# Kernel tuning notes

Hardware: AMD Instinct MI355X
Metric: run time of the kernel (lower is better)

Reference implementation:

```python
import jax, jax.numpy as jnp
import numpy as np
from jax import lax

B, IN_C, H, W = 2, 256, 80, 80
OUT_C = 256
INTER = IN_C // 16          # 16
C4 = IN_C // 4              # 64
K = 3
DIL = [7, 5, 2, 1]
PADS = [(K + (K - 1) * (d - 1)) // 2 for d in DIL]  # same-padding per module formula


def conv2d(x, w, b=None, pad=0, dil=1, groups=1):
    out = lax.conv_general_dilated(
        x, w, (1, 1), [(pad, pad), (pad, pad)], rhs_dilation=(dil, dil),
        dimension_numbers=('NCHW', 'OIHW', 'NCHW'), feature_group_count=groups)
    if b is not None:
        out = out + b[None, :, None, None]
    return out


def bnorm(x, g, b, eps=1e-3):
    # BatchNorm2d in training mode (fresh module): biased batch stats, eps=0.001
    m = x.mean((0, 2, 3), keepdims=True)
    v = x.var((0, 2, 3), keepdims=True)
    return (x - m) * lax.rsqrt(v + eps) * g[None, :, None, None] + b[None, :, None, None]


def gnorm(x, g, b, groups=4, eps=1e-5):
    Bb, C, Hh, Ww = x.shape
    xr = x.reshape(Bb, groups, C // groups, Hh, Ww)
    m = xr.mean((2, 3, 4), keepdims=True)
    v = xr.var((2, 3, 4), keepdims=True)
    xr = (xr - m) * lax.rsqrt(v + eps)
    return xr.reshape(Bb, C, Hh, Ww) * g[None, :, None, None] + b[None, :, None, None]


def setup_inputs() -> dict:
    keys = jax.random.split(jax.random.key(0), 40)

    def w_init(k, shape):
        fan = float(np.prod(shape[1:]))
        return jax.random.normal(k, shape, jnp.float32) / np.sqrt(fan)

    d = {}
    d['z'] = jax.random.normal(keys[0], (B, IN_C, H, W), jnp.float32)
    for i in range(4):  # depthwise dilated convs: (C4, 1, 3, 3)
        d[f'w_at{i}'] = w_init(keys[1 + 2 * i], (C4, 1, K, K))
        d[f'b_at{i}'] = jax.random.normal(keys[2 + 2 * i], (C4,), jnp.float32) * 0.02
    d['gn_w'] = 1.0 + 0.05 * jax.random.normal(keys[9], (IN_C,), jnp.float32)
    d['gn_b'] = 0.05 * jax.random.normal(keys[10], (IN_C,), jnp.float32)
    d['conv_w'] = w_init(keys[11], (IN_C, IN_C, 1, 1))
    d['conv_b'] = jax.random.normal(keys[12], (IN_C,), jnp.float32) * 0.02
    d['c5a_w'] = w_init(keys[13], (INTER, IN_C, 3, 3))
    d['bn5a_w'] = 1.0 + 0.05 * jax.random.normal(keys[14], (INTER,), jnp.float32)
    d['bn5a_b'] = 0.05 * jax.random.normal(keys[15], (INTER,), jnp.float32)
    d['c5c_w'] = w_init(keys[16], (INTER, IN_C, 3, 3))
    d['bn5c_w'] = 1.0 + 0.05 * jax.random.normal(keys[17], (INTER,), jnp.float32)
    d['bn5c_b'] = 0.05 * jax.random.normal(keys[18], (INTER,), jnp.float32)
    d['pq_w'] = w_init(keys[19], (INTER // 8, INTER, 1, 1))
    d['pq_b'] = jax.random.normal(keys[20], (INTER // 8,), jnp.float32) * 0.02
    d['pk_w'] = w_init(keys[21], (INTER // 8, INTER, 1, 1))
    d['pk_b'] = jax.random.normal(keys[22], (INTER // 8,), jnp.float32) * 0.02
    d['pv_w'] = w_init(keys[23], (INTER, INTER, 1, 1))
    d['pv_b'] = jax.random.normal(keys[24], (INTER,), jnp.float32) * 0.02
    d['pa_gamma'] = 0.5 * jnp.ones((1,), jnp.float32)  # nonzero so attn path is exercised
    d['ca_gamma'] = 0.5 * jnp.ones((1,), jnp.float32)
    d['c5b_w'] = w_init(keys[25], (INTER, INTER, 3, 3))
    d['bn5b_w'] = 1.0 + 0.05 * jax.random.normal(keys[26], (INTER,), jnp.float32)
    d['bn5b_b'] = 0.05 * jax.random.normal(keys[27], (INTER,), jnp.float32)
    d['c5d_w'] = w_init(keys[28], (INTER, INTER, 3, 3))
    d['bn5d_w'] = 1.0 + 0.05 * jax.random.normal(keys[29], (INTER,), jnp.float32)
    d['bn5d_b'] = 0.05 * jax.random.normal(keys[30], (INTER,), jnp.float32)
    d['c6_w'] = w_init(keys[31], (OUT_C, INTER, 1, 1))
    d['c6_b'] = jax.random.normal(keys[32], (OUT_C,), jnp.float32) * 0.02
    return d


def reference(z, w_at0, b_at0, w_at1, b_at1, w_at2, b_at2, w_at3, b_at3,
              gn_w, gn_b, conv_w, conv_b,
              c5a_w, bn5a_w, bn5a_b, c5c_w, bn5c_w, bn5c_b,
              pq_w, pq_b, pk_w, pk_b, pv_w, pv_b, pa_gamma, ca_gamma,
              c5b_w, bn5b_w, bn5b_b, c5d_w, bn5d_w, bn5d_b, c6_w, c6_b):
    parts = jnp.split(z, 4, axis=1)
    ws = [w_at0, w_at1, w_at2, w_at3]
    bs = [b_at0, b_at1, b_at2, b_at3]
    zs = [conv2d(parts[i], ws[i], bs[i], pad=PADS[i], dil=DIL[i], groups=C4)
          for i in range(4)]
    zc = jnp.concatenate(zs, axis=1)
    zc = jax.nn.gelu(conv2d(gnorm(zc, gn_w, gn_b), conv_w, conv_b), approximate=False)

    # --- DABlock ---
    feat1 = jax.nn.relu(bnorm(conv2d(zc, c5a_w, pad=1), bn5a_w, bn5a_b))
    Bb, C, Hh, Ww = feat1.shape
    N = Hh * Ww
    # PAM: full HWxHW attention
    q = conv2d(feat1, pq_w, pq_b).reshape(Bb, -1, N)   # (B, C//8, N)
    k = conv2d(feat1, pk_w, pk_b).reshape(Bb, -1, N)
    v = conv2d(feat1, pv_w, pv_b).reshape(Bb, C, N)
    energy = jnp.einsum('bcn,bcm->bnm', q, k)          # (B, N, N)
    att = jax.nn.softmax(energy, axis=-1)
    pa = jnp.einsum('bcm,bnm->bcn', v, att).reshape(Bb, C, Hh, Ww)
    pa = pa_gamma * pa + feat1
    pa_conv = jax.nn.relu(bnorm(conv2d(pa, c5b_w, pad=1), bn5b_w, bn5b_b))

    feat2 = jax.nn.relu(bnorm(conv2d(zc, c5c_w, pad=1), bn5c_w, bn5c_b))
    # CAM: CxC attention
    xf = feat2.reshape(Bb, C, N)
    e = jnp.einsum('bcn,bdn->bcd', xf, xf)             # (B, C, C)
    e = e.max(-1, keepdims=True) - e
    att_c = jax.nn.softmax(e, axis=-1)
    ca = jnp.einsum('bcd,bdn->bcn', att_c, xf).reshape(Bb, C, Hh, Ww)
    ca = ca_gamma * ca + feat2
    ca_conv = jax.nn.relu(bnorm(conv2d(ca, c5d_w, pad=1), bn5d_w, bn5d_b))

    # Dropout2d(p=0.05) is identity in eval mode
    out = jax.nn.relu(conv2d(pa_conv + ca_conv, c6_w, c6_b))
    return out
```

## Files before the change

### kernel.cpp

```cpp
#include <hip/hip_runtime.h>
#include <math.h>

#define HW 6400

typedef __attribute__((ext_vector_type(8))) short bf16x8;
typedef __attribute__((ext_vector_type(4))) float f32x4;

__device__ __forceinline__ float wredsum(float v){
  #pragma unroll
  for (int o = 32; o; o >>= 1) v += __shfl_xor(v, o);
  return v;
}

__device__ __forceinline__ unsigned short f2bf(float f){
  unsigned int u = __float_as_uint(f);
  u += 0x7FFF + ((u >> 16) & 1);
  return (unsigned short)(u >> 16);
}

__device__ __forceinline__ float bf2f(unsigned short s){
  return __uint_as_float((unsigned int)s << 16);
}

__device__ __forceinline__ unsigned int cvt_pk_bf16(float lo, float hi){
  unsigned int r;
  asm("v_cvt_pk_bf16_f32 %0, %1, %2" : "=v"(r) : "v"(lo), "v"(hi));
  return r;
}

__device__ __forceinline__ float gelu(float v){
  return 0.5f * v * (1.f + erff(v * 0.70710678118f));
}

__global__ __launch_bounds__(256) void k_prep(
    const float* __restrict__ wa, const float* __restrict__ wc,
    const float* __restrict__ wb, const float* __restrict__ wd,
    const float* __restrict__ cw, const float* __restrict__ gn_sc,
    const float* __restrict__ cb,
    unsigned short* __restrict__ wbbf,
    unsigned short* __restrict__ cwbf, float* __restrict__ cbp,
    unsigned short* __restrict__ wbbf2){
  int bx = blockIdx.x;
  int tid = threadIdx.x;
  if (bx < 288){
    int i = bx * 256 + tid;
    if (i < 73728){
      int j = i & 7, l = (i >> 3) & 63, f = (i >> 9) & 1, ss = i >> 10;
      int k = ss * 32 + (l >> 4) * 8 + j;
      int off = k >> 8, ic = k & 255;
      int oc = f * 16 + (l & 15);
      float v = (oc < 16) ? wa[(oc * 256 + ic) * 9 + off]
                          : wc[((oc - 16) * 256 + ic) * 9 + off];
      wbbf[i] = f2bf(v);
    }
  } else if (bx < 800){
    int i = (bx - 288) * 256 + tid;
    int b = i >> 16, r = i & 65535;
    int j = r & 7, l = (r >> 3) & 63, f = (r >> 9) & 15, ss = r >> 13;
    int ic = ss * 32 + (l >> 4) * 8 + j;
    int oc = f * 16 + (l & 15);
    cwbf[i] = f2bf(cw[oc * 256 + ic] * gn_sc[(b * 256 + ic) * 2]);
  } else if (bx < 832){
    int bb = bx - 800;
    int b = bb >> 4;
    int oc = (bb & 15) * 16 + (tid >> 4);
    int cp = tid & 15;
    float s2 = 0.f;
    #pragma unroll
    for (int k = 0; k < 16; k++){
      int c = cp * 16 + k;
      s2 += cw[oc * 256 + c] * gn_sc[(b * 256 + c) * 2 + 1];
    }
    s2 += __shfl_xor(s2, 1); s2 += __shfl_xor(s2, 2);
    s2 += __shfl_xor(s2, 4); s2 += __shfl_xor(s2, 8);
    if (cp == 0) cbp[b * 256 + oc] = cb[oc] + s2;
  } else {
    int i = (bx - 832) * 256 + tid;
    if (i < 9216){
      int j = i & 7, l = (i >> 3) & 63, f = (i >> 9) & 1, off = i >> 10;
      int kk = (l >> 4) * 8 + j;
      int oc = f * 16 + (l & 15);
      float v = 0.f;
      if (oc < 16 && kk < 16)        v = wb[(oc * 16 + kk) * 9 + off];
      else if (oc >= 16 && kk >= 16) v = wd[((oc - 16) * 16 + (kk - 16)) * 9 + off];
      wbbf2[i] = f2bf(v);
    }
  }
}

__global__ __launch_bounds__(256) void k_dwt(
    const float* __restrict__ z,
    const float* __restrict__ w0, const float* __restrict__ b0,
    const float* __restrict__ w1, const float* __restrict__ b1,
    const float* __restrict__ w2, const float* __restrict__ b2,
    const float* __restrict__ w3, const float* __restrict__ b3,
    unsigned short* __restrict__ zbf, float* __restrict__ gnpart){
  __shared__ unsigned short lt[64][66];
  int tid = threadIdx.x;
  int g = blockIdx.y, b = blockIdx.z;
  int p0 = blockIdx.x * 64;
  int lane = tid & 63, s = tid >> 6;
  int pix = p0 + lane;
  int h = pix / 80, w = pix % 80;
  const float* wp; const float* bp; int d;
  if (g == 0){ wp = w0; bp = b0; d = 7; }
  else if (g == 1){ wp = w1; bp = b1; d = 5; }
  else if (g == 2){ wp = w2; bp = b2; d = 2; }
  else            { wp = w3; bp = b3; d = 1; }
  int offr[9]; float msk[9];
  #pragma unroll
  for (int kh = 0; kh < 3; kh++){
    #pragma unroll
    for (int kw = 0; kw < 3; kw++){
      bool ok = ((unsigned)(h + (kh - 1) * d) < 80u) && ((unsigned)(w + (kw - 1) * d) < 80u);
      offr[kh * 3 + kw] = ok ? ((kh - 1) * d * 80 + (kw - 1) * d) : 0;
      msk[kh * 3 + kw] = ok ? 1.f : 0.f;
    }
  }
  const float* zb = z + (size_t)(b * 256 + g * 64) * HW + pix;
  for (int j = 0; j < 16; j++){
    int cl = s * 16 + j;
    const float* zin = zb + (size_t)cl * HW;
    const float* wr = wp + cl * 9;
    float acc = bp[cl];
    #pragma unroll
    for (int k = 0; k < 9; k++) acc = fmaf(wr[k], zin[offr[k]] * msk[k], acc);
    float S = wredsum(acc), Q = wredsum(acc * acc);
    if (lane == 0){
      int cg = b * 256 + g * 64 + cl;
      gnpart[(cg * 100 + blockIdx.x) * 2]     = S;
      gnpart[(cg * 100 + blockIdx.x) * 2 + 1] = Q;
    }
    lt[lane][cl] = f2bf(acc);
  }
  __syncthreads();
  int pr = tid >> 2, q = tid & 3;
  const unsigned short* src = &lt[pr][q * 16];
  unsigned int tmp[8];
  #pragma unroll
  for (int u = 0; u < 8; u++) tmp[u] = *(const unsigned int*)(src + u * 2);
  uint4 v0 = make_uint4(tmp[0], tmp[1], tmp[2], tmp[3]);
  uint4 v1 = make_uint4(tmp[4], tmp[5], tmp[6], tmp[7]);
  unsigned short* dst = zbf + ((size_t)b * HW + p0 + pr) * 256 + g * 64 + q * 16;
  *(uint4*)dst = v0;
  *(uint4*)(dst + 8) = v1;
}

__global__ __launch_bounds__(256) void k_gnfin(
    const float* __restrict__ gnpart, const float* __restrict__ gn_w,
    const float* __restrict__ gn_b, float* __restrict__ gn_sc){
  int tid = threadIdx.x; int bg = blockIdx.x;
  int b = bg >> 2, g = bg & 3;
  size_t base = (size_t)(b * 256 + g * 64) * 200;
  float S = 0.f, Q = 0.f;
  for (int i = tid; i < 6400; i += 256){
    S += gnpart[base + 2 * i];
    Q += gnpart[base + 2 * i + 1];
  }
  S = wredsum(S); Q = wredsum(Q);
  __shared__ float l[8];
  int lane = tid & 63, wid = tid >> 6;
  if (lane == 0){ l[wid] = S; l[4 + wid] = Q; }
  __syncthreads();
  float SS = l[0] + l[1] + l[2] + l[3];
  float QQ = l[4] + l[5] + l[6] + l[7];
  float M = 64.f * HW;
  float mean = SS / M;
  float var = QQ / M - mean * mean;
  float rstd = rsqrtf(var + 1e-5f);
  if (tid < 64){
    int c = g * 64 + tid;
    float sc = gn_w[c] * rstd;
    float sh = gn_b[c] - mean * sc;
    gn_sc[(b * 256 + c) * 2] = sc;
    gn_sc[(b * 256 + c) * 2 + 1] = sh;
  }
}

__global__ __launch_bounds__(256) void k_conv1_mfma(
    const unsigned short* __restrict__ zbf,
    const unsigned short* __restrict__ cwbf,
    const float* __restrict__ cbp,
    unsigned short* __restrict__ zbfT){
  __shared__ __align__(16) unsigned char lmem[64 * 512];
  unsigned short* lda = (unsigned short*)lmem;
  unsigned short* lout = (unsigned short*)lmem;
  int tid = threadIdx.x;
  int p0 = blockIdx.x * 64, ocg = blockIdx.y, b = blockIdx.z;
  #pragma unroll
  for (int k = 0; k < 8; k++){
    int m = tid + k * 256;
    int i = m >> 5, c = m & 31;
    bf16x8 val = *(const bf16x8*)(zbf + ((size_t)b * HW + p0 + i) * 256 + c * 8);
    *(bf16x8*)(lda + i * 256 + (c ^ (i & 7)) * 8) = val;
  }
  __syncthreads();
  int wv = tid >> 6, l = tid & 63;
  int row = l & 15, kg = l >> 4;
  int i = wv * 16 + row;
  f32x4 acc0 = {0.f,0.f,0.f,0.f}, acc1 = {0.f,0.f,0.f,0.f};
  f32x4 acc2 = {0.f,0.f,0.f,0.f}, acc3 = {0.f,0.f,0.f,0.f};
  const unsigned short* wp = cwbf + (size_t)b * 65536 + (ocg * 4) * 512 + l * 8;
  #pragma unroll
  for (int s = 0; s < 8; s++){
    int c = s * 4 + kg;
    bf16x8 a = *(const bf16x8*)(lda + i * 256 + (c ^ (i & 7)) * 8);
    const unsigned short* wps = wp + s * 8192;
    bf16x8 b0 = *(const bf16x8*)(wps);
    bf16x8 b1 = *(const bf16x8*)(wps + 512);
    bf16x8 b2 = *(const bf16x8*)(wps + 1024);
    bf16x8 b3 = *(const bf16x8*)(wps + 1536);
    acc0 = __builtin_amdgcn_mfma_f32_16x16x32_bf16(a, b0, acc0, 0, 0, 0);
    acc1 = __builtin_amdgcn_mfma_f32_16x16x32_bf16(a, b1, acc1, 0, 0, 0);
    acc2 = __builtin_amdgcn_mfma_f32_16x16x32_bf16(a, b2, acc2, 0, 0, 0);
    acc3 = __builtin_amdgcn_mfma_f32_16x16x32_bf16(a, b3, acc3, 0, 0, 0);
  }
  __syncthreads();
  const float* cbb = cbp + b * 256 + ocg * 64;
  int oc_l = l & 15;
  int pl = wv * 16 + kg * 4;
  float bs0 = cbb[oc_l], bs1 = cbb[16 + oc_l], bs2 = cbb[32 + oc_l], bs3 = cbb[48 + oc_l];
  #pragma unroll
  for (int r = 0; r < 4; r++){
    lout[(pl + r) * 72 + oc_l]      = f2bf(gelu(acc0[r] + bs0));
    lout[(pl + r) * 72 + 16 + oc_l] = f2bf(gelu(acc1[r] + bs1));
    lout[(pl + r) * 72 + 32 + oc_l] = f2bf(gelu(acc2[r] + bs2));
    lout[(pl + r) * 72 + 48 + oc_l] = f2bf(gelu(acc3[r] + bs3));
  }
  __syncthreads();
  int pix = tid >> 2, q = tid & 3;
  unsigned short* dst = zbfT + ((size_t)b * HW + p0 + pix) * 256 + ocg * 64 + q * 16;
  const unsigned short* src = lout + pix * 72 + q * 16;
  *(uint4*)dst       = *(const uint4*)src;
  *(uint4*)(dst + 8) = *(const uint4*)(src + 8);
}

__device__ __forceinline__ void c5_gload(bf16x8* r, const unsigned short* zbase,
    int p0, int irow, int c31, const int* hh, const int* ww, int off){
  int dy = off / 3 - 1, dx = off % 3 - 1;
  int doff = dy * 80 + dx;
  #pragma unroll
  for (int k = 0; k < 8; k++){
    int op = p0 + irow + k * 8;
    bool v = ((unsigned)(hh[k] + dy) < 80u) && ((unsigned)(ww[k] + dx) < 80u);
    int sp = v ? (op + doff) : op;
    bf16x8 val = *(const bf16x8*)(zbase + (size_t)sp * 256 + c31 * 8);
    if (!v) val = (bf16x8){0, 0, 0, 0, 0, 0, 0, 0};
    r[k] = val;
  }
}

__global__ __launch_bounds__(256) void k_conv5ac2(
    const unsigned short* __restrict__ zbfT,
    const unsigned short* __restrict__ wbbf,
    float* __restrict__ fpre, float* __restrict__ bnpart){
  __shared__ __align__(16) unsigned short lda[2][64 * 256];
  int tid = threadIdx.x;
  int och = blockIdx.y, b = blockIdx.z;
  int p0 = blockIdx.x * 64;
  int irow = tid >> 5, c31 = tid & 31;
  int hh[8], ww[8];
  #pragma unroll
  for (int k = 0; k < 8; k++){
    int op = p0 + irow + k * 8;
    hh[k] = op / 80; ww[k] = op % 80;
  }
  const unsigned short* zbase = zbfT + (size_t)b * HW * 256;
  bf16x8 r[8];
  c5_gload(r, zbase, p0, irow, c31, hh, ww, 0);
  #pragma unroll
  for (int k = 0; k < 8; k++){
    int i = irow + k * 8;
    *(bf16x8*)(lda[0] + i * 256 + (c31 ^ (i & 7)) * 8) = r[k];
  }
  c5_gload(r, zbase, p0, irow, c31, hh, ww, 1);
  int wv = tid >> 6, l = tid & 63;
  int lrow = l & 15, kg = l >> 4;
  int li = wv * 16 + lrow;
  f32x4 acc = {0.f, 0.f, 0.f, 0.f};
  for (int off = 0; off < 9; off++){
    __syncthreads();
    int buf = off & 1;
    const unsigned short* wp = wbbf + (size_t)off * 8192 + och * 512 + l * 8;
    #pragma unroll
    for (int s = 0; s < 8; s++){
      int cc = s * 4 + kg;
      bf16x8 a = *(const bf16x8*)(lda[buf] + li * 256 + (cc ^ (li & 7)) * 8);
      bf16x8 bb = *(const bf16x8*)(wp + s * 1024);
      acc = __builtin_amdgcn_mfma_f32_16x16x32_bf16(a, bb, acc, 0, 0, 0);
    }
    if (off + 1 < 9){
      #pragma unroll
      for (int k = 0; k < 8; k++){
        int i = irow + k * 8;
        *(bf16x8*)(lda[buf ^ 1] + i * 256 + (c31 ^ (i & 7)) * 8) = r[k];
      }
      if (off + 2 < 9) c5_gload(r, zbase, p0, irow, c31, hh, ww, off + 2);
    }
  }
  __syncthreads();
  float* lout = (float*)lda;
  int ocl = l & 15;
  int pl = wv * 16 + kg * 4;
  #pragma unroll
  for (int rr = 0; rr < 4; rr++) lout[ocl * 68 + pl + rr] = acc[rr];
  __syncthreads();
  int oc = tid >> 4, px = (tid & 15) * 4;
  float4 v = *(float4*)(lout + oc * 68 + px);
  *(float4*)(fpre + ((size_t)(b * 32 + och * 16 + oc)) * HW + p0 + px) = v;
  float S = v.x + v.y + v.z + v.w;
  float Q = v.x * v.x + v.y * v.y + v.z * v.z + v.w * v.w;
  #pragma unroll
  for (int o2 = 1; o2 < 16; o2 <<= 1){ S += __shfl_xor(S, o2); Q += __shfl_xor(Q, o2); }
  if ((tid & 15) == 0){
    int ocg = och * 16 + oc;
    bnpart[ocg * 400 + (b * 100 + blockIdx.x) * 2]     = S;
    bnpart[ocg * 400 + (b * 100 + blockIdx.x) * 2 + 1] = Q;
  }
}

__global__ __launch_bounds__(256) void k_featqkv(
    const float* __restrict__ fpre, const float* __restrict__ bnpart,
    const float* __restrict__ w1, const float* __restrict__ b1,
    const float* __restrict__ w2, const float* __restrict__ b2,
    const float* __restrict__ pqw, const float* __restrict__ pqb,
    const float* __restrict__ pkw, const float* __restrict__ pkb,
    const float* __restrict__ pvw, const float* __restrict__ pvb,
    float* __restrict__ feat, float* __restrict__ qkvT,
    float* __restrict__ cam_part){
  __shared__ float lS[8][32], lQ[8][32], lsc[64];
  __shared__ float lf2[256][17];
  int tid = threadIdx.x; int b = blockIdx.y;
  {
    int oc = tid & 31, sl = tid >> 5;
    float S = 0.f, Q = 0.f;
    for (int i = sl; i < 200; i += 8){
      S += bnpart[oc * 400 + i * 2];
      Q += bnpart[oc * 400 + i * 2 + 1];
    }
    lS[sl][oc] = S; lQ[sl][oc] = Q;
    __syncthreads();
    if (tid < 32){
      float SS = 0.f, QQ = 0.f;
      #pragma unroll
      for (int s = 0; s < 8; s++){ SS += lS[s][tid]; QQ += lQ[s][tid]; }
      float M = 2.f * HW;
      float mean = SS / M, var = QQ / M - mean * mean;
      float rstd = rsqrtf(var + 1e-3f);
      float w  = (tid < 16) ? w1[tid] : w2[tid - 16];
      float bb = (tid < 16) ? b1[tid] : b2[tid - 16];
      float sc = w * rstd;
      lsc[tid * 2] = sc; lsc[tid * 2 + 1] = bb - mean * sc;
    }
    __syncthreads();
  }
  int n = blockIdx.x * 256 + tid;
  float f1[16], f2[16];
  #pragma unroll
  for (int c = 0; c < 16; c++){
    float v1 = fpre[(b * 32 + c) * HW + n] * lsc[c * 2] + lsc[c * 2 + 1];
    f1[c] = fmaxf(v1, 0.f);
    float v2 = fpre[(b * 32 + 16 + c) * HW + n] * lsc[(16 + c) * 2] + lsc[(16 + c) * 2 + 1];
    f2[c] = fmaxf(v2, 0.f);
    feat[(b * 32 + c) * HW + n] = f1[c];
    feat[(b * 32 + 16 + c) * HW + n] = f2[c];
    lf2[tid][c] = f2[c];
  }
  float* o = qkvT + ((size_t)b * HW + n) * 20;
  #pragma unroll
  for (int j = 0; j < 2; j++){
    float q = pqb[j], k = pkb[j];
    #pragma unroll
    for (int c = 0; c < 16; c++){ q += pqw[j * 16 + c] * f1[c]; k += pkw[j * 16 + c] * f1[c]; }
    o[j] = q; o[2 + j] = k;
  }
  #pragma unroll
  for (int j = 0; j < 16; j++){
    float v = pvb[j];
    #pragma unroll
    for (int c = 0; c < 16; c++) v += pvw[j * 16 + c] * f1[c];
    o[4 + j] = v;
  }
  __syncthreads();
  int cc = tid >> 4, dd = tid & 15;
  float s = 0.f;
  #pragma unroll 4
  for (int p = 0; p < 256; p++) s = fmaf(lf2[p][cc], lf2[p][dd], s);
  cam_part[((size_t)blockIdx.x * 2 + b) * 256 + tid] = s;
}

__global__ __launch_bounds__(256) void k_pam_a(
    const float* __restrict__ qkvT, float* __restrict__ part){
  __shared__ __align__(16) float lk0[800];
  __shared__ __align__(16) float lk1[800];
  __shared__ __align__(16) unsigned short lvb[16][808];
  __shared__ float lred[4];
  int tid = threadIdx.x;
  int mc = blockIdx.y, b = blockIdx.z;
  float sqm = 0.f;
  for (int m = tid; m < 800; m += 256){
    const float* kv = qkvT + ((size_t)b * HW + mc * 800 + m) * 20;
    float4 a0 = *(const float4*)kv;
    lk0[m] = a0.z; lk1[m] = a0.w;
    sqm = fmaxf(sqm, a0.z * a0.z + a0.w * a0.w);
    float4 v0 = *(const float4*)(kv + 4);
    float4 v1 = *(const float4*)(kv + 8);
    float4 v2 = *(const float4*)(kv + 12);
    float4 v3 = *(const float4*)(kv + 16);
    lvb[0][m]  = f2bf(v0.x); lvb[1][m]  = f2bf(v0.y);
    lvb[2][m]  = f2bf(v0.z); lvb[3][m]  = f2bf(v0.w);
    lvb[4][m]  = f2bf(v1.x); lvb[5][m]  = f2bf(v1.y);
    lvb[6][m]  = f2bf(v1.z); lvb[7][m]  = f2bf(v1.w);
    lvb[8][m]  = f2bf(v2.x); lvb[9][m]  = f2bf(v2.y);
    lvb[10][m] = f2bf(v2.z); lvb[11][m] = f2bf(v2.w);
    lvb[12][m] = f2bf(v3.x); lvb[13][m] = f2bf(v3.y);
    lvb[14][m] = f2bf(v3.z); lvb[15][m] = f2bf(v3.w);
  }
  #pragma unroll
  for (int o = 32; o; o >>= 1) sqm = fmaxf(sqm, __shfl_xor(sqm, o));
  int lane = tid & 63, wid = tid >> 6;
  if (lane == 0) lred[wid] = sqm;
  __syncthreads();
  float kmax = sqrtf(fmaxf(fmaxf(lred[0], lred[1]), fmaxf(lred[2], lred[3])));
  int wv = tid >> 6, l = tid & 63;
  int row = l & 15, kg = l >> 4;
  int n = blockIdx.x * 64 + wv * 16 + row;
  const float* qp = qkvT + ((size_t)b * HW + n) * 20;
  float q0 = qp[0], q1 = qp[1];
  float mxr = sqrtf(q0 * q0 + q1 * q1) * kmax;
  f32x4 acc = {0.f, 0.f, 0.f, 0.f};
  float zp = 0.f;
  for (int t = 0; t < 25; t++){
    int m0 = t * 32 + kg * 8;
    float4 k0a = *(const float4*)&lk0[m0];
    float4 k0b = *(const float4*)&lk0[m0 + 4];
    float4 k1a = *(const float4*)&lk1[m0];
    float4 k1b = *(const float4*)&lk1[m0 + 4];
    float p0 = __expf(fmaf(q0, k0a.x, q1 * k1a.x) - mxr);
    float p1 = __expf(fmaf(q0, k0a.y, q1 * k1a.y) - mxr);
    float p2 = __expf(fmaf(q0, k0a.z, q1 * k1a.z) - mxr);
    float p3 = __expf(fmaf(q0, k0a.w, q1 * k1a.w) - mxr);
    float p4 = __expf(fmaf(q0, k0b.x, q1 * k1b.x) - mxr);
    float p5 = __expf(fmaf(q0, k0b.y, q1 * k1b.y) - mxr);
    float p6 = __expf(fmaf(q0, k0b.z, q1 * k1b.z) - mxr);
    float p7 = __expf(fmaf(q0, k0b.w, q1 * k1b.w) - mxr);
    zp += ((p0 + p1) + (p2 + p3)) + ((p4 + p5) + (p6 + p7));
    union { unsigned int u[4]; bf16x8 v; } pk;
    pk.u[0] = cvt_pk_bf16(p0, p1);
    pk.u[1] = cvt_pk_bf16(p2, p3);
    pk.u[2] = cvt_pk_bf16(p4, p5);
    pk.u[3] = cvt_pk_bf16(p6, p7);
    bf16x8 vb = *(const bf16x8*)&lvb[row][m0];
    acc = __builtin_amdgcn_mfma_f32_16x16x32_bf16(pk.v, vb, acc, 0, 0, 0);
  }
  zp += __shfl_xor(zp, 16);
  zp += __shfl_xor(zp, 32);
  float* pp = part + ((size_t)(b * 8 + mc) * 18) * HW;
  if (kg == 0){ pp[n] = mxr; pp[HW + n] = zp; }
  int c = l & 15;
  int nr = blockIdx.x * 64 + wv * 16 + (l >> 4) * 4;
  *(f32x4*)&pp[(size_t)(2 + c) * HW + nr] = acc;
}

__global__ __launch_bounds__(256) void k_merge(
    const float* __restrict__ part, const float* __restrict__ feat,
    const float* __restrict__ cam_part,
    const float* __restrict__ pa_g, const float* __restrict__ ca_g,
    unsigned short* __restrict__ mc){
  __shared__ float le[256];
  __shared__ float lsm[8][16];
  int tid = threadIdx.x; int y = blockIdx.y, b = blockIdx.z;
  int n = blockIdx.x * 256 + tid;
  union { unsigned short s[8]; uint4 u; } rowo;
  if (y < 2){
    int c0 = y * 8;
    float mxs[8]; float mx = -1e30f;
    #pragma unroll
    for (int m8 = 0; m8 < 8; m8++){
      mxs[m8] = part[((size_t)(b * 8 + m8) * 18) * HW + n];
      mx = fmaxf(mx, mxs[m8]);
    }
    float Z = 0.f, a[8];
    #pragma unroll
    for (int j = 0; j < 8; j++) a[j] = 0.f;
    #pragma unroll
    for (int m8 = 0; m8 < 8; m8++){
      const float* pp = part + ((size_t)(b * 8 + m8) * 18) * HW + n;
      float r = __expf(mxs[m8] - mx);
      Z += pp[HW] * r;
      #pragma unroll
      for (int j = 0; j < 8; j++) a[j] += pp[(size_t)(2 + c0 + j) * HW] * r;
    }
    float invp = pa_g[0] / Z;
    #pragma unroll
    for (int j = 0; j < 8; j++)
      rowo.s[j] = f2bf(fmaf(a[j], invp, feat[(b * 32 + c0 + j) * HW + n]));
    *(uint4*)(mc + ((size_t)b * HW + n) * 32 + c0) = rowo.u;
  } else {
    int c0 = (y - 2) * 8;
    float s = 0.f;
    #pragma unroll
    for (int blk = 0; blk < 25; blk++)
      s += cam_part[((size_t)blk * 2 + b) * 256 + tid];
    le[tid] = s;
    __syncthreads();
    if (tid < 8){
      int c = c0 + tid;
      float rr[16]; float mn = 1e30f;
      #pragma unroll
      for (int d = 0; d < 16; d++){ rr[d] = le[c * 16 + d]; mn = fminf(mn, rr[d]); }
      float p[16]; float ssum = 0.f;
      #pragma unroll
      for (int d = 0; d < 16; d++){ p[d] = __expf(mn - rr[d]); ssum += p[d]; }
      float inv = ca_g[0] / ssum;
      #pragma unroll
      for (int d = 0; d < 16; d++) lsm[tid][d] = p[d] * inv;
    }
    __syncthreads();
    float f2[16];
    #pragma unroll
    for (int c = 0; c < 16; c++) f2[c] = feat[(b * 32 + 16 + c) * HW + n];
    #pragma unroll
    for (int j = 0; j < 8; j++){
      float s2 = 0.f;
      #pragma unroll
      for (int d = 0; d < 16; d++) s2 = fmaf(lsm[j][d], f2[d], s2);
      rowo.s[j] = f2bf(s2 + f2[c0 + j]);
    }
    *(uint4*)(mc + ((size_t)b * HW + n) * 32 + 16 + c0) = rowo.u;
  }
}

__global__ __launch_bounds__(256) void k_conv5bd_mfma(
    const unsigned short* __restrict__ mc,
    const unsigned short* __restrict__ wbbf2,
    unsigned short* __restrict__ bdb, float* __restrict__ bnpart){
  __shared__ __align__(16) unsigned short lda[9 * 2048];
  __shared__ float lS[8][32], lQ[8][32];
  int tid = threadIdx.x;
  int b = blockIdx.z;
  int p0 = blockIdx.x * 64;
  int i = tid >> 2, q = tid & 3;
  int op = p0 + i;
  int h = op / 80, w = op % 80;
  const unsigned short* mb = mc + (size_t)b * HW * 32;
  #pragma unroll
  for (int off = 0; off < 9; off++){
    int dy = off / 3 - 1, dx = off % 3 - 1;
    bool v = ((unsigned)(h + dy) < 80u) && ((unsigned)(w + dx) < 80u);
    int sp = v ? (op + dy * 80 + dx) : op;
    bf16x8 val = *(const bf16x8*)(mb + (size_t)sp * 32 + q * 8);
    if (!v) val = (bf16x8){0, 0, 0, 0, 0, 0, 0, 0};
    int c8 = ((i & 1) * 4 + q) ^ ((i >> 1) & 7);
    *(bf16x8*)(lda + off * 2048 + (i >> 1) * 64 + c8 * 8) = val;
  }
  __syncthreads();
  int wv = tid >> 6, l = tid & 63;
  int row = l & 15, kg = l >> 4;
  int i2 = wv * 16 + row;
  f32x4 acc0 = {0.f, 0.f, 0.f, 0.f};
  f32x4 acc1 = {0.f, 0.f, 0.f, 0.f};
  #pragma unroll
  for (int off = 0; off < 9; off++){
    int c8 = ((i2 & 1) * 4 + kg) ^ ((i2 >> 1) & 7);
    bf16x8 a = *(const bf16x8*)(lda + off * 2048 + (i2 >> 1) * 64 + c8 * 8);
    bf16x8 b0 = *(const bf16x8*)(wbbf2 + off * 1024 + l * 8);
    bf16x8 b1 = *(const bf16x8*)(wbbf2 + off * 1024 + 512 + l * 8);
    acc0 = __builtin_amdgcn_mfma_f32_16x16x32_bf16(a, b0, acc0, 0, 0, 0);
    acc1 = __builtin_amdgcn_mfma_f32_16x16x32_bf16(a, b1, acc1, 0, 0, 0);
  }
  __syncthreads();
  float* lout = (float*)lda;
  int ocl = l & 15;
  int pl = wv * 16 + kg * 4;
  #pragma unroll
  for (int r = 0; r < 4; r++){
    lout[(pl + r) * 34 + ocl]      = acc0[r];
    lout[(pl + r) * 34 + 16 + ocl] = acc1[r];
  }
  __syncthreads();
  {
    int pix = tid >> 2, qq = tid & 3;
    const float* src = lout + pix * 34 + qq * 8;
    union { unsigned int u[4]; bf16x8 v; } pk;
    pk.u[0] = cvt_pk_bf16(src[0], src[1]);
    pk.u[1] = cvt_pk_bf16(src[2], src[3]);
    pk.u[2] = cvt_pk_bf16(src[4], src[5]);
    pk.u[3] = cvt_pk_bf16(src[6], src[7]);
    *(bf16x8*)(bdb + ((size_t)b * HW + p0 + pix) * 32 + qq * 8) = pk.v;
  }
  {
    int oc = tid & 31, grp = tid >> 5;
    float S = 0.f, Q = 0.f;
    #pragma unroll
    for (int r = 0; r < 8; r++){
      float v = lout[(grp * 8 + r) * 34 + oc];
      S += v; Q += v * v;
    }
    lS[grp][oc] = S; lQ[grp][oc] = Q;
  }
  __syncthreads();
  if (tid < 32){
    float S = 0.f, Q = 0.f;
    #pragma unroll
    for (int g2 = 0; g2 < 8; g2++){ S += lS[g2][tid]; Q += lQ[g2][tid]; }
    bnpart[tid * 400 + (b * 100 + blockIdx.x) * 2]     = S;
    bnpart[tid * 400 + (b * 100 + blockIdx.x) * 2 + 1] = Q;
  }
}

__global__ __launch_bounds__(256) void k_c6(
    const unsigned short* __restrict__ bdb, const float* __restrict__ bnpart,
    const float* __restrict__ w1, const float* __restrict__ b1,
    const float* __restrict__ w2, const float* __restrict__ b2,
    const float* __restrict__ w6, const float* __restrict__ b6,
    float* __restrict__ out){
  __shared__ float lS[8][32], lQ[8][32], lsc[64];
  int tid = threadIdx.x; int og = blockIdx.y * 16, b = blockIdx.z;
  {
    int oc = tid & 31, sl = tid >> 5;
    float S = 0.f, Q = 0.f;
    for (int i = sl; i < 200; i += 8){
      S += bnpart[oc * 400 + i * 2];
      Q += bnpart[oc * 400 + i * 2 + 1];
    }
    lS[sl][oc] = S; lQ[sl][oc] = Q;
    __syncthreads();
    if (tid < 32){
      float SS = 0.f, QQ = 0.f;
      #pragma unroll
      for (int s = 0; s < 8; s++){ SS += lS[s][tid]; QQ += lQ[s][tid]; }
      float M = 2.f * HW;
      float mean = SS / M, var = QQ / M - mean * mean;
      float rstd = rsqrtf(var + 1e-3f);
      float w  = (tid < 16) ? w1[tid] : w2[tid - 16];
      float bb = (tid < 16) ? b1[tid] : b2[tid - 16];
      float sc = w * rstd;
      lsc[tid * 2] = sc; lsc[tid * 2 + 1] = bb - mean * sc;
    }
    __syncthreads();
  }
  int n = blockIdx.x * 256 + tid;
  const unsigned short* rowp = bdb + ((size_t)b * HW + n) * 32;
  union { bf16x8 v[4]; unsigned short s[32]; } r;
  r.v[0] = *(const bf16x8*)(rowp);
  r.v[1] = *(const bf16x8*)(rowp + 8);
  r.v[2] = *(const bf16x8*)(rowp + 16);
  r.v[3] = *(const bf16x8*)(rowp + 24);
  float x[16];
  #pragma unroll
  for (int c = 0; c < 16; c++){
    float v1 = bf2f((unsigned short)r.s[c]) * lsc[c * 2] + lsc[c * 2 + 1];
    float v2 = bf2f((unsigned short)r.s[16 + c]) * lsc[(16 + c) * 2] + lsc[(16 + c) * 2 + 1];
    x[c] = fmaxf(v1, 0.f) + fmaxf(v2, 0.f);
  }
  #pragma unroll
  for (int o = 0; o < 16; o++){
    float a = b6[og + o];
    #pragma unroll
    for (int c = 0; c < 16; c++) a += w6[(og + o) * 16 + c] * x[c];
    out[(b * 256 + og + o) * HW + n] = fmaxf(a, 0.f);
  }
}

extern "C" void kernel_launch(void* const* d_in, const int* in_sizes, int n_in,
                              void* d_out, int out_size, void* d_ws, size_t ws_size,
                              hipStream_t stream){
  const float* z      = (const float*)d_in[0];
  const float* w_at0  = (const float*)d_in[1];
  const float* b_at0  = (const float*)d_in[2];
  const float* w_at1  = (const float*)d_in[3];
  const float* b_at1  = (const float*)d_in[4];
  const float* w_at2  = (const float*)d_in[5];
  const float* b_at2  = (const float*)d_in[6];
  const float* w_at3  = (const float*)d_in[7];
  const float* b_at3  = (const float*)d_in[8];
  const float* gn_w   = (const float*)d_in[9];
  const float* gn_b   = (const float*)d_in[10];
  const float* conv_w = (const float*)d_in[11];
  const float* conv_b = (const float*)d_in[12];
  const float* c5a_w  = (const float*)d_in[13];
  const float* bn5a_w = (const float*)d_in[14];
  const float* bn5a_b = (const float*)d_in[15];
  const float* c5c_w  = (const float*)d_in[16];
  const float* bn5c_w = (const float*)d_in[17];
  const float* bn5c_b = (const float*)d_in[18];
  const float* pq_w   = (const float*)d_in[19];
  const float* pq_b   = (const float*)d_in[20];
  const float* pk_w   = (const float*)d_in[21];
  const float* pk_b   = (const float*)d_in[22];
  const float* pv_w   = (const float*)d_in[23];
  const float* pv_b   = (const float*)d_in[24];
  const float* pa_g   = (const float*)d_in[25];
  const float* ca_g   = (const float*)d_in[26];
  const float* c5b_w  = (const float*)d_in[27];
  const float* bn5b_w = (const float*)d_in[28];
  const float* bn5b_b = (const float*)d_in[29];
  const float* c5d_w  = (const float*)d_in[30];
  const float* bn5d_w = (const float*)d_in[31];
  const float* bn5d_b = (const float*)d_in[32];
  const float* c6_w   = (const float*)d_in[33];
  const float* c6_b   = (const float*)d_in[34];

  float* ws = (float*)d_ws;
  unsigned short* ZBF    = (unsigned short*)ws;
  unsigned short* ZC2BFT = (unsigned short*)(ws + 1638400);
  unsigned short* CWBF   = (unsigned short*)(ws + 3276800);
  float* CBP     = ws + 3407872;
  float* FPRE    = ws + 3408384;
  float* FEAT    = FPRE + 409600;
  float* QKVT    = FEAT + 409600;
  unsigned short* MC  = (unsigned short*)(QKVT + 256000);
  unsigned short* BDB = (unsigned short*)(QKVT + 256000 + 204800);
  float* ST      = QKVT + 256000 + 409600;
  float* GN_SC    = ST;
  float* CAM_PART = ST + 1024;
  float* GN_PART  = ST + 14336;
  float* BNA_PART = ST + 116736;
  float* BNB_PART = ST + 129536;
  unsigned short* WBBF  = (unsigned short*)(ST + 142336);
  unsigned short* WBBF2 = (unsigned short*)(ST + 179200);
  float* PART = ws;

  k_dwt<<<dim3(100, 4, 2), 256, 0, stream>>>(z, w_at0, b_at0, w_at1, b_at1,
                                             w_at2, b_at2, w_at3, b_at3, ZBF, GN_PART);
  k_gnfin<<<8, 256, 0, stream>>>(GN_PART, gn_w, gn_b, GN_SC);
  k_prep<<<868, 256, 0, stream>>>(c5a_w, c5c_w, c5b_w, c5d_w, conv_w, GN_SC, conv_b,
                                  WBBF, CWBF, CBP, WBBF2);
  k_conv1_mfma<<<dim3(100, 4, 2), 256, 0, stream>>>(ZBF, CWBF, CBP, ZC2BFT);
  k_conv5ac2<<<dim3(100, 2, 2), 256, 0, stream>>>(ZC2BFT, WBBF, FPRE, BNA_PART);
  k_featqkv<<<dim3(25, 2), 256, 0, stream>>>(FPRE, BNA_PART, bn5a_w, bn5a_b,
                                             bn5c_w, bn5c_b, pq_w, pq_b, pk_w, pk_b,
                                             pv_w, pv_b, FEAT, QKVT, CAM_PART);
  k_pam_a<<<dim3(100, 8, 2), 256, 0, stream>>>(QKVT, PART);
  k_merge<<<dim3(25, 4, 2), 256, 0, stream>>>(PART, FEAT, CAM_PART, pa_g, ca_g, MC);
  k_conv5bd_mfma<<<dim3(100, 1, 2), 256, 0, stream>>>(MC, WBBF2, BDB, BNB_PART);
  k_c6<<<dim3(25, 16, 2), 256, 0, stream>>>(BDB, BNB_PART, bn5b_w, bn5b_b,
                                            bn5d_w, bn5d_b, c6_w, c6_b, (float*)d_out);
}
```

Before: 127.8 us.

## Fuse GroupNorm finalize into weight prep and vectorize PAM K/V staging

Removes the separate k_gnfin launch. Each k_prep block that needs GroupNorm statistics now reduces the partial sums itself and folds scale and shift into the conv weights and bias. This saves a kernel launch and a dependency step, but the same 12800-element reduction is repeated in hundreds of blocks, adding redundant global reads. Separately, k_pam_a now stages K and V with each thread handling four contiguous positions, using packed bf16 conversion and vector LDS stores in place of scalar stores.

```diff
diff --git a/kernel.cpp b/kernel.cpp
--- a/kernel.cpp
+++ b/kernel.cpp
@@ -35,11 +35,14 @@
 __global__ __launch_bounds__(256) void k_prep(
     const float* __restrict__ wa, const float* __restrict__ wc,
     const float* __restrict__ wb, const float* __restrict__ wd,
-    const float* __restrict__ cw, const float* __restrict__ gn_sc,
+    const float* __restrict__ cw, const float* __restrict__ gnpart,
+    const float* __restrict__ gn_w, const float* __restrict__ gn_b,
     const float* __restrict__ cb,
     unsigned short* __restrict__ wbbf,
     unsigned short* __restrict__ cwbf, float* __restrict__ cbp,
     unsigned short* __restrict__ wbbf2){
+  __shared__ float lred[8];
+  __shared__ float lmv[4][2];
   int bx = blockIdx.x;
   int tid = threadIdx.x;
   if (bx < 288){
@@ -56,20 +59,65 @@
   } else if (bx < 800){
     int i = (bx - 288) * 256 + tid;
     int b = i >> 16, r = i & 65535;
-    int j = r & 7, l = (r >> 3) & 63, f = (r >> 9) & 15, ss = r >> 13;
+    int ss = r >> 13;
+    int g = ss >> 1;
+    size_t base = (size_t)(b * 256 + g * 64) * 200;
+    float S = 0.f, Q = 0.f;
+    for (int t = tid; t < 6400; t += 256){
+      S += gnpart[base + 2 * t];
+      Q += gnpart[base + 2 * t + 1];
+    }
+    S = wredsum(S); Q = wredsum(Q);
+    int lane = tid & 63, wid = tid >> 6;
+    if (lane == 0){ lred[wid] = S; lred[4 + wid] = Q; }
+    __syncthreads();
+    if (tid == 0){
+      float SS = lred[0] + lred[1] + lred[2] + lred[3];
+      float QQ = lred[4] + lred[5] + lred[6] + lred[7];
+      float M = 64.f * HW;
+      float mean = SS / M;
+      float var = QQ / M - mean * mean;
+      lmv[0][0] = mean; lmv[0][1] = rsqrtf(var + 1e-5f);
+    }
+    __syncthreads();
+    float rstd = lmv[0][1];
+    int j = r & 7, l = (r >> 3) & 63, f = (r >> 9) & 15;
     int ic = ss * 32 + (l >> 4) * 8 + j;
     int oc = f * 16 + (l & 15);
-    cwbf[i] = f2bf(cw[oc * 256 + ic] * gn_sc[(b * 256 + ic) * 2]);
+    cwbf[i] = f2bf(cw[oc * 256 + ic] * gn_w[ic] * rstd);
   } else if (bx < 832){
     int bb = bx - 800;
     int b = bb >> 4;
+    for (int g = 0; g < 4; g++){
+      size_t base = (size_t)(b * 256 + g * 64) * 200;
+      float S = 0.f, Q = 0.f;
+      for (int t = tid; t < 6400; t += 256){
+        S += gnpart[base + 2 * t];
+        Q += gnpart[base + 2 * t + 1];
+      }
+      S = wredsum(S); Q = wredsum(Q);
+      int lane = tid & 63, wid = tid >> 6;
+      if (lane == 0){ lred[wid] = S; lred[4 + wid] = Q; }
+      __syncthreads();
+      if (tid == 0){
+        float SS = lred[0] + lred[1] + lred[2] + lred[3];
+        float QQ = lred[4] + lred[5] + lred[6] + lred[7];
+        float M = 64.f * HW;
+        float mean = SS / M;
+        float var = QQ / M - mean * mean;
+        lmv[g][0] = mean; lmv[g][1] = rsqrtf(var + 1e-5f);
+      }
+      __syncthreads();
+    }
     int oc = (bb & 15) * 16 + (tid >> 4);
     int cp = tid & 15;
     float s2 = 0.f;
     #pragma unroll
     for (int k = 0; k < 16; k++){
       int c = cp * 16 + k;
-      s2 += cw[oc * 256 + c] * gn_sc[(b * 256 + c) * 2 + 1];
+      int g = c >> 6;
+      float sh = gn_b[c] - lmv[g][0] * gn_w[c] * lmv[g][1];
+      s2 += cw[oc * 256 + c] * sh;
     }
     s2 += __shfl_xor(s2, 1); s2 += __shfl_xor(s2, 2);
     s2 += __shfl_xor(s2, 4); s2 += __shfl_xor(s2, 8);
@@ -146,37 +194,6 @@
   *(uint4*)(dst + 8) = v1;
 }
 
-__global__ __launch_bounds__(256) void k_gnfin(
-    const float* __restrict__ gnpart, const float* __restrict__ gn_w,
-    const float* __restrict__ gn_b, float* __restrict__ gn_sc){
-  int tid = threadIdx.x; int bg = blockIdx.x;
-  int b = bg >> 2, g = bg & 3;
-  size_t base = (size_t)(b * 256 + g * 64) * 200;
-  float S = 0.f, Q = 0.f;
-  for (int i = tid; i < 6400; i += 256){
-    S += gnpart[base + 2 * i];
-    Q += gnpart[base + 2 * i + 1];
-  }
-  S = wredsum(S); Q = wredsum(Q);
-  __shared__ float l[8];
-  int lane = tid & 63, wid = tid >> 6;
-  if (lane == 0){ l[wid] = S; l[4 + wid] = Q; }
-  __syncthreads();
-  float SS = l[0] + l[1] + l[2] + l[3];
-  float QQ = l[4] + l[5] + l[6] + l[7];
-  float M = 64.f * HW;
-  float mean = SS / M;
-  float var = QQ / M - mean * mean;
-  float rstd = rsqrtf(var + 1e-5f);
-  if (tid < 64){
-    int c = g * 64 + tid;
-    float sc = gn_w[c] * rstd;
-    float sh = gn_b[c] - mean * sc;
-    gn_sc[(b * 256 + c) * 2] = sc;
-    gn_sc[(b * 256 + c) * 2 + 1] = sh;
-  }
-}
-
 __global__ __launch_bounds__(256) void k_conv1_mfma(
     const unsigned short* __restrict__ zbf,
     const unsigned short* __restrict__ cwbf,
@@ -398,23 +415,44 @@
   int tid = threadIdx.x;
   int mc = blockIdx.y, b = blockIdx.z;
   float sqm = 0.f;
-  for (int m = tid; m < 800; m += 256){
-    const float* kv = qkvT + ((size_t)b * HW + mc * 800 + m) * 20;
-    float4 a0 = *(const float4*)kv;
-    lk0[m] = a0.z; lk1[m] = a0.w;
-    sqm = fmaxf(sqm, a0.z * a0.z + a0.w * a0.w);
-    float4 v0 = *(const float4*)(kv + 4);
-    float4 v1 = *(const float4*)(kv + 8);
-    float4 v2 = *(const float4*)(kv + 12);
-    float4 v3 = *(const float4*)(kv + 16);
-    lvb[0][m]  = f2bf(v0.x); lvb[1][m]  = f2bf(v0.y);
-    lvb[2][m]  = f2bf(v0.z); lvb[3][m]  = f2bf(v0.w);
-    lvb[4][m]  = f2bf(v1.x); lvb[5][m]  = f2bf(v1.y);
-    lvb[6][m]  = f2bf(v1.z); lvb[7][m]  = f2bf(v1.w);
-    lvb[8][m]  = f2bf(v2.x); lvb[9][m]  = f2bf(v2.y);
-    lvb[10][m] = f2bf(v2.z); lvb[11][m] = f2bf(v2.w);
-    lvb[12][m] = f2bf(v3.x); lvb[13][m] = f2bf(v3.y);
-    lvb[14][m] = f2bf(v3.z); lvb[15][m] = f2bf(v3.w);
+  if (tid < 200){
+    int m0 = tid * 4;
+    const float* kv0 = qkvT + ((size_t)b * HW + mc * 800 + m0) * 20;
+    float k0v[4], k1v[4];
+    float va[4][8];
+    #pragma unroll
+    for (int k = 0; k < 4; k++){
+      const float* kv = kv0 + k * 20;
+      float4 a0 = *(const float4*)kv;
+      k0v[k] = a0.z; k1v[k] = a0.w;
+      sqm = fmaxf(sqm, a0.z * a0.z + a0.w * a0.w);
+      float4 v0 = *(const float4*)(kv + 4);
+      float4 v1 = *(const float4*)(kv + 8);
+      va[k][0] = v0.x; va[k][1] = v0.y; va[k][2] = v0.z; va[k][3] = v0.w;
+      va[k][4] = v1.x; va[k][5] = v1.y; va[k][6] = v1.z; va[k][7] = v1.w;
+    }
+    *(float4*)&lk0[m0] = make_float4(k0v[0], k0v[1], k0v[2], k0v[3]);
+    *(float4*)&lk1[m0] = make_float4(k1v[0], k1v[1], k1v[2], k1v[3]);
+    #pragma unroll
+    for (int c = 0; c < 8; c++){
+      unsigned int u0 = cvt_pk_bf16(va[0][c], va[1][c]);
+      unsigned int u1 = cvt_pk_bf16(va[2][c], va[3][c]);
+      *(uint2*)&lvb[c][m0] = make_uint2(u0, u1);
+    }
+    #pragma unroll
+    for (int k = 0; k < 4; k++){
+      const float* kv = kv0 + k * 20;
+      float4 v2 = *(const float4*)(kv + 12);
+      float4 v3 = *(const float4*)(kv + 16);
+      va[k][0] = v2.x; va[k][1] = v2.y; va[k][2] = v2.z; va[k][3] = v2.w;
+      va[k][4] = v3.x; va[k][5] = v3.y; va[k][6] = v3.z; va[k][7] = v3.w;
+    }
+    #pragma unroll
+    for (int c = 0; c < 8; c++){
+      unsigned int u0 = cvt_pk_bf16(va[0][c], va[1][c]);
+      unsigned int u1 = cvt_pk_bf16(va[2][c], va[3][c]);
+      *(uint2*)&lvb[8 + c][m0] = make_uint2(u0, u1);
+    }
   }
   #pragma unroll
   for (int o = 32; o; o >>= 1) sqm = fmaxf(sqm, __shfl_xor(sqm, o));
@@ -713,7 +751,6 @@
   unsigned short* MC  = (unsigned short*)(QKVT + 256000);
   unsigned short* BDB = (unsigned short*)(QKVT + 256000 + 204800);
   float* ST      = QKVT + 256000 + 409600;
-  float* GN_SC    = ST;
   float* CAM_PART = ST + 1024;
   float* GN_PART  = ST + 14336;
   float* BNA_PART = ST + 116736;
@@ -724,9 +761,8 @@
 
   k_dwt<<<dim3(100, 4, 2), 256, 0, stream>>>(z, w_at0, b_at0, w_at1, b_at1,
                                              w_at2, b_at2, w_at3, b_at3, ZBF, GN_PART);
-  k_gnfin<<<8, 256, 0, stream>>>(GN_PART, gn_w, gn_b, GN_SC);
-  k_prep<<<868, 256, 0, stream>>>(c5a_w, c5c_w, c5b_w, c5d_w, conv_w, GN_SC, conv_b,
-                                  WBBF, CWBF, CBP, WBBF2);
+  k_prep<<<868, 256, 0, stream>>>(c5a_w, c5c_w, c5b_w, c5d_w, conv_w, GN_PART,
+                                  gn_w, gn_b, conv_b, WBBF, CWBF, CBP, WBBF2);
   k_conv1_mfma<<<dim3(100, 4, 2), 256, 0, stream>>>(ZBF, CWBF, CBP, ZC2BFT);
   k_conv5ac2<<<dim3(100, 2, 2), 256, 0, stream>>>(ZC2BFT, WBBF, FPRE, BNA_PART);
   k_featqkv<<<dim3(25, 2), 256, 0, stream>>>(FPRE, BNA_PART, bn5a_w, bn5a_b,
```

After: 135.5 us. +6.0%, slower.
